# Optimization experiments

Hardware: AMD Instinct MI355X
Metric: run time of the kernel (lower is better)

The kernel has to match this reference:

```python
import jax, jax.numpy as jnp
import numpy as np

H, FF = 4096, 14336   # hidden size, SwiGLU intermediate size
B, S = 4, 2048        # batch, sequence length


def setup_inputs() -> dict:
    key = jax.random.key(0)
    ks = jax.random.split(key, 7)
    x = jax.random.normal(ks[0], (B, S, H), dtype=jnp.float32)
    # Ternary weights: values in {-1, 0, +1}
    gate_t = jax.random.randint(ks[1], (FF, H), -1, 2, dtype=jnp.int32)
    up_t = jax.random.randint(ks[2], (FF, H), -1, 2, dtype=jnp.int32)
    down_t = jax.random.randint(ks[3], (H, FF), -1, 2, dtype=jnp.int32)
    # Per-output-row scales (positive, realistic quantization scale magnitudes)
    gate_s = jax.random.uniform(ks[4], (FF,), jnp.float32, 0.01, 0.1)
    up_s = jax.random.uniform(ks[5], (FF,), jnp.float32, 0.01, 0.1)
    down_s = jax.random.uniform(ks[6], (H,), jnp.float32, 0.01, 0.1)
    return {"x": x, "gate_t": gate_t, "up_t": up_t, "down_t": down_t,
            "gate_s": gate_s, "up_s": up_s, "down_s": down_s}


def reference(x, gate_t, up_t, down_t, gate_s, up_s, down_s):
    # SwiGLU forward with on-the-fly ternary dequant, matching
    # TernaryExpertModule.forward (output_proj=None).
    Bb, Ss, Hh = x.shape
    x_flat = x.reshape(Bb * Ss, Hh)                         # [BS, H]
    gate_w = gate_t.astype(jnp.float32) * gate_s[:, None]   # [FF, H]
    up_w = up_t.astype(jnp.float32) * up_s[:, None]         # [FF, H]
    down_w = down_t.astype(jnp.float32) * down_s[:, None]   # [H, FF]
    gate_out = x_flat @ gate_w.T                            # [BS, FF]
    up_out = x_flat @ up_w.T                                # [BS, FF]
    hidden = jax.nn.silu(gate_out) * up_out                 # [BS, FF]
    out_flat = hidden @ down_w.T                            # [BS, H]
    return out_flat.reshape(Bb, Ss, -1)
```

## Files before the change

kernel.cpp:

```cpp
#include <hip/hip_runtime.h>
#include <stdint.h>

#define H_DIM   4096
#define FF_DIM  14336
#define M_TOK   8192
#define KC1     (H_DIM / 32)
#define KC2     (FF_DIM / 32)
#define NC1     (H_DIM / 64)

typedef unsigned short ushort_t;
typedef __attribute__((ext_vector_type(8)))  short bf16x8;
typedef __attribute__((ext_vector_type(4)))  float f32x4;
typedef __attribute__((ext_vector_type(4)))  int   i32x4;

__device__ __forceinline__ unsigned short f2bf(float f) {
    union { float f; uint32_t u; } v; v.f = f;
    uint32_t r = v.u + 0x7FFFu + ((v.u >> 16) & 1u);
    return (unsigned short)(r >> 16);
}
__device__ __forceinline__ unsigned short t2bf(int v) {
    unsigned int mag = (v & 1) ? 0x3F80u : 0u;
    unsigned int sgn = ((unsigned int)v >> 16) & 0x8000u;
    return (unsigned short)(mag | sgn);
}
__device__ __forceinline__ bf16x8 pack_f8(f32x4 a, f32x4 b) {
    bf16x8 o;
    o[0]=(short)f2bf(a[0]); o[1]=(short)f2bf(a[1]); o[2]=(short)f2bf(a[2]); o[3]=(short)f2bf(a[3]);
    o[4]=(short)f2bf(b[0]); o[5]=(short)f2bf(b[1]); o[6]=(short)f2bf(b[2]); o[7]=(short)f2bf(b[3]);
    return o;
}
__device__ __forceinline__ bf16x8 pack_t8(i32x4 a, i32x4 b) {
    bf16x8 o;
    o[0]=(short)t2bf(a[0]); o[1]=(short)t2bf(a[1]); o[2]=(short)t2bf(a[2]); o[3]=(short)t2bf(a[3]);
    o[4]=(short)t2bf(b[0]); o[5]=(short)t2bf(b[1]); o[6]=(short)t2bf(b[2]); o[7]=(short)t2bf(b[3]);
    return o;
}
__device__ __forceinline__ int pack4(int a, int b, int c, int d) {
    return (a & 255) | ((b & 255) << 8) | ((c & 255) << 16) | ((d & 255) << 24);
}

#define GLDS16(gp, lp) __builtin_amdgcn_global_load_lds( \
    (__attribute__((address_space(1))) void*)(gp),       \
    (__attribute__((address_space(3))) void*)(lp), 16, 0, 0)

#define WAITVM8  asm volatile("s_waitcnt vmcnt(8)" ::: "memory")
#define WAITVM4  asm volatile("s_waitcnt vmcnt(4)" ::: "memory")
#define WAITVM0  asm volatile("s_waitcnt vmcnt(0)" ::: "memory")
#define SBAR     asm volatile("s_barrier" ::: "memory")


template<int K, bool TERN>
__global__ __launch_bounds__(256)
void k_cvt_lds(const void* __restrict__ inv, unsigned short* __restrict__ out) {
    constexpr int KC = K / 32;
    constexpr int CP = K / 64;
    __shared__ int sm[128][68];
    const int b   = blockIdx.x;
    const int t   = b / CP;
    const int cp  = b % CP;
    const int tid = threadIdx.x;
    const int rr  = tid >> 4;
    const int c4  = (tid & 15) * 4;
    const int k0  = cp * 64;

    const int* in = (const int*)inv;
    #pragma unroll
    for (int p = 0; p < 8; ++p) {
        const int row = p * 16 + rr;
        *(i32x4*)&sm[row][c4] = *(const i32x4*)(in + (size_t)(t * 128 + row) * K + k0 + c4);
    }
    __syncthreads();
    #pragma unroll
    for (int p = 0; p < 4; ++p) {
        const int idx = p * 256 + tid;
        const int cc  = idx >> 9;
        const int f   = (idx >> 6) & 7;
        const int l   = idx & 63;
        const int row = f * 16 + (l & 15);
        const int kl  = cc * 32 + (l >> 4) * 8;
        bf16x8 o;
        if (TERN) {
            i32x4 a = *(const i32x4*)&sm[row][kl];
            i32x4 bq = *(const i32x4*)&sm[row][kl + 4];
            o = pack_t8(a, bq);
        } else {
            f32x4 a = *(const f32x4*)&sm[row][kl];
            f32x4 bq = *(const f32x4*)&sm[row][kl + 4];
            o = pack_f8(a, bq);
        }
        *(bf16x8*)(out + (((size_t)t * KC + (cp * 2 + cc)) * 8 + f) * 512 + (size_t)l * 8) = o;
    }
}

__global__ __launch_bounds__(256)
void k_amax(const float* __restrict__ x, float* __restrict__ sx, float* __restrict__ rsx) {
    const int row  = blockIdx.x * 4 + (threadIdx.x >> 6);
    const int lane = threadIdx.x & 63;
    const f32x4* p = (const f32x4*)(x + (size_t)row * H_DIM);
    float m = 0.f;
    #pragma unroll 4
    for (int i = lane; i < H_DIM / 4; i += 64) {
        f32x4 v = p[i];
        m = fmaxf(m, fmaxf(fmaxf(fabsf(v[0]), fabsf(v[1])), fmaxf(fabsf(v[2]), fabsf(v[3]))));
    }
    #pragma unroll
    for (int o = 32; o; o >>= 1) m = fmaxf(m, __shfl_xor(m, o, 64));
    if (lane == 0) {
        sx[row]  = m * (1.f / 127.f);
        rsx[row] = m > 0.f ? 127.f / m : 0.f;
    }
}

template<int K, bool TERN>
__global__ __launch_bounds__(256)
void k_cvt_i8(const void* __restrict__ inv, const float* __restrict__ rsx,
              char* __restrict__ out) {
    constexpr int CP = K / 64;
    __shared__ int sm[128][68];
    const int b   = blockIdx.x;
    const int t   = b / CP;
    const int cp  = b % CP;
    const int tid = threadIdx.x;
    const int rr  = tid >> 4;
    const int c4  = (tid & 15) * 4;

    const int* in = (const int*)inv;
    #pragma unroll
    for (int p = 0; p < 8; ++p) {
        const int row = p * 16 + rr;
        *(i32x4*)&sm[row][c4] = *(const i32x4*)(in + (size_t)(t * 128 + row) * K + cp * 64 + c4);
    }
    __syncthreads();
    #pragma unroll
    for (int p = 0; p < 2; ++p) {
        const int pos = p * 256 + tid;
        const int f = pos >> 6, l = pos & 63;
        const int row = f * 16 + (l & 15);
        const int kb  = (l >> 4) * 16;
        i32x4 o;
        if constexpr (TERN) {
            #pragma unroll
            for (int q = 0; q < 4; ++q)
                o[q] = pack4(sm[row][kb + q * 4], sm[row][kb + q * 4 + 1],
                             sm[row][kb + q * 4 + 2], sm[row][kb + q * 4 + 3]);
        } else {
            const float rs = rsx[t * 128 + row];
            #pragma unroll
            for (int q = 0; q < 4; ++q) {
                const float* fp = (const float*)&sm[row][kb + q * 4];
                o[q] = pack4(__float2int_rn(fp[0] * rs), __float2int_rn(fp[1] * rs),
                             __float2int_rn(fp[2] * rs), __float2int_rn(fp[3] * rs));
            }
        }
        *(i32x4*)(out + ((size_t)t * CP + cp) * 8192 + f * 1024 + (size_t)l * 16) = o;
    }
}

__global__ __launch_bounds__(512, 2)
void k_gemm1_i8(const char* __restrict__ xq,
                const char* __restrict__ gq, const char* __restrict__ uq,
                const float* __restrict__ sxp,
                const float* __restrict__ gs, const float* __restrict__ us,
                ushort_t* __restrict__ hid)
{
    __shared__ char lds[65536];
    const int tid  = threadIdx.x;
    const int lane = tid & 63;
    const int wv   = tid >> 6;
    const int wr   = wv >> 1;
    const int wc   = wv & 1;
    const int l15  = lane & 15;
    const int lq   = lane >> 4;

    const int bid = blockIdx.x;
    const int bmt = bid & 31;
    const int bnt = bid >> 5;

    const char* xa0 = xq + (size_t)(bmt * 2)     * NC1 * 8192;
    const char* xa1 = xq + (size_t)(bmt * 2 + 1) * NC1 * 8192;
    const char* gbb = gq + (size_t)bnt * NC1 * 8192;
    const char* ubb = uq + (size_t)bnt * NC1 * 8192;

    i32x4 accg[4][4] = {};
    i32x4 accu[4][4] = {};

#define STAGE1(h) { char* sl_ = lds + ((h) & 1) * 32768;                     \
    GLDS16(xa0 + (size_t)(h) * 8192 + tid * 16, sl_ + tid * 16);             \
    GLDS16(xa1 + (size_t)(h) * 8192 + tid * 16, sl_ + 8192  + tid * 16);     \
    GLDS16(gbb + (size_t)(h) * 8192 + tid * 16, sl_ + 16384 + tid * 16);     \
    GLDS16(ubb + (size_t)(h) * 8192 + tid * 16, sl_ + 24576 + tid * 16); }

#define G1BODY(WAITOP, DO_STAGE)                                                    \
  {                                                                                 \
    if (DO_STAGE) STAGE1(H + 1);                                                    \
    WAITOP;              \
    SBAR;                                        \
    char* slot = lds + (H & 1) * 32768;                                             \
    const char* Ab = slot + (wr >> 1) * 8192 + ((wr & 1) * 4) * 1024 + lane * 16;   \
    const char* Gb = slot + 16384 + (wc * 4) * 1024 + lane * 16;                    \
    const char* Ub = slot + 24576 + (wc * 4) * 1024 + lane * 16;                    \
    i32x4 af[4], gf[4], uf[4];                                                      \
    _Pragma("unroll")                                                               \
    for (int m = 0; m < 4; m++) af[m] = *(const i32x4*)(Ab + m * 1024);             \
    _Pragma("unroll")                                                               \
    for (int n = 0; n < 4; n++) {                                                   \
        gf[n] = *(const i32x4*)(Gb + n * 1024);                                     \
        uf[n] = *(const i32x4*)(Ub + n * 1024);                                     \
    }                                                                               \
    __builtin_amdgcn_s_setprio(1);                                                  \
    _Pragma("unroll")                                                               \
    for (int m = 0; m < 4; m++)                                                     \
      _Pragma("unroll")                                                             \
      for (int n = 0; n < 4; n++)                                                   \
        accg[m][n] = __builtin_amdgcn_mfma_i32_16x16x64_i8(af[m], gf[n], accg[m][n], 0, 0, 0); \
    _Pragma("unroll")                                                               \
    for (int m = 0; m < 4; m++)                                                     \
      _Pragma("unroll")                                                             \
      for (int n = 0; n < 4; n++)                                                   \
        accu[m][n] = __builtin_amdgcn_mfma_i32_16x16x64_i8(af[m], uf[n], accu[m][n], 0, 0, 0); \
    __builtin_amdgcn_s_setprio(0);                                                  \
    SBAR;                \
  }

    STAGE1(0);
    int H = 0;
    for (; H < NC1 - 1; ++H) G1BODY(WAITVM4, 1);
    G1BODY(WAITVM0, 0);
#undef G1BODY
#undef STAGE1

    const int bm0 = bmt * 256;
    const int bn0 = bnt * 128;
    float sxv[4][4];
    #pragma unroll
    for (int m = 0; m < 4; m++) {
        const int rb = bm0 + wr * 64 + m * 16 + lq * 4;
        #pragma unroll
        for (int r = 0; r < 4; r++) sxv[m][r] = sxp[rb + r];
    }
    #pragma unroll
    for (int n = 0; n < 4; n++) {
        const int gcol = bn0 + wc * 64 + n * 16 + l15;
        const float sg = gs[gcol];
        const float su = us[gcol];
        const int c  = gcol >> 5;
        const int lp = ((gcol & 31) >> 3) * 16;
        const int e  = gcol & 7;
        #pragma unroll
        for (int m = 0; m < 4; m++) {
            const int rb = bm0 + wr * 64 + m * 16 + lq * 4;
            #pragma unroll
            for (int r = 0; r < 4; r++) {
                const int row = rb + r;
                float g = (float)accg[m][n][r] * (sxv[m][r] * sg);
                float u = (float)accu[m][n][r] * (sxv[m][r] * su);
                float hv = g * (1.0f / (1.0f + __expf(-g))) * u;
                const int t = row >> 7;
                const int f = (row >> 4) & 7;
                const int l = (row & 15) + lp;
                hid[(((size_t)t * KC2 + c) * 8 + f) * 512 + l * 8 + e] = f2bf(hv);
            }
        }
    }
}

__global__ __launch_bounds__(512, 2)
void k_gemm2_8p(const ushort_t* __restrict__ hid, const ushort_t* __restrict__ db,
                const float* __restrict__ dsc, float* __restrict__ out)
{
    __shared__ ushort_t lds[65536];
    const int tid  = threadIdx.x;
    const int lane = tid & 63;
    const int wv   = tid >> 6;
    const int wr   = wv >> 2;
    const int wc   = wv & 3;
    const int l15  = lane & 15;
    const int lq   = lane >> 4;

    const int bid = blockIdx.x;
    const int bmt = bid & 31;
    const int bnt = bid >> 5;

    const ushort_t* ha0 = hid + ((size_t)(bmt * 2)     * KC2) * 4096;
    const ushort_t* ha1 = hid + ((size_t)(bmt * 2 + 1) * KC2) * 4096;
    const ushort_t* db0 = db  + ((size_t)(bnt * 2)     * KC2) * 4096;
    const ushort_t* db1 = db  + ((size_t)(bnt * 2 + 1) * KC2) * 4096;

    f32x4 acc[8][4] = {};

    #pragma unroll
    for (int h = 0; h < 3; ++h) {
        ushort_t* sl = lds + h * 16384;
        GLDS16(ha0 + (size_t)h * 4096 + tid * 8, sl + tid * 8);
        GLDS16(ha1 + (size_t)h * 4096 + tid * 8, sl + 4096 + tid * 8);
        GLDS16(db0 + (size_t)h * 4096 + tid * 8, sl + 8192 + tid * 8);
        GLDS16(db1 + (size_t)h * 4096 + tid * 8, sl + 12288 + tid * 8);
    }

#define G2_HALF(WAITOP, DO_ISSUE)                                                  \
  {                                                                                \
    ushort_t* slot = lds + (H & 3) * 16384;                                        \
    const ushort_t* Ab = slot + wr * 4096 + lane * 8;                              \
    const ushort_t* Bb = slot + 8192 + (wc >> 1) * 4096 + ((wc & 1) * 4) * 512 + lane * 8; \
    WAITOP;                                                                        \
    SBAR;                                                                          \
    bf16x8 af[4], bfv[4];                                                          \
    _Pragma("unroll")                                                              \
    for (int m = 0; m < 4; m++) af[m] = *(const bf16x8*)(Ab + m * 512);            \
    _Pragma("unroll")                                                              \
    for (int n = 0; n < 4; n++) bfv[n] = *(const bf16x8*)(Bb + n * 512);           \
    if (DO_ISSUE) {                                                                \
      const int Hp = H + 3;                                                        \
      ushort_t* sp = lds + (Hp & 3) * 16384;                                       \
      GLDS16(ha0 + (size_t)Hp * 4096 + tid * 8, sp + tid * 8);                     \
      GLDS16(ha1 + (size_t)Hp * 4096 + tid * 8, sp + 4096 + tid * 8);              \
    }                                                                              \
    __builtin_amdgcn_s_setprio(1);                                                 \
    _Pragma("unroll")                                                              \
    for (int m = 0; m < 4; m++)                                                    \
      _Pragma("unroll")                                                            \
      for (int n = 0; n < 4; n++)                                                  \
        acc[m][n] = __builtin_amdgcn_mfma_f32_16x16x32_bf16(af[m], bfv[n], acc[m][n], 0, 0, 0); \
    __builtin_amdgcn_s_setprio(0);                                                 \
    SBAR;                                                                          \
    bf16x8 af2[4];                                                                 \
    _Pragma("unroll")                                                              \
    for (int m = 0; m < 4; m++) af2[m] = *(const bf16x8*)(Ab + (4 + m) * 512);     \
    if (DO_ISSUE) {                                                                \
      const int Hp = H + 3;                                                        \
      ushort_t* sp = lds + (Hp & 3) * 16384;                                       \
      GLDS16(db0 + (size_t)Hp * 4096 + tid * 8, sp + 8192 + tid * 8);              \
      GLDS16(db1 + (size_t)Hp * 4096 + tid * 8, sp + 12288 + tid * 8);             \
    }                                                                              \
    __builtin_amdgcn_s_setprio(1);                                                 \
    _Pragma("unroll")                                                              \
    for (int m = 0; m < 4; m++)                                                    \
      _Pragma("unroll")                                                            \
      for (int n = 0; n < 4; n++)                                                  \
        acc[4 + m][n] = __builtin_amdgcn_mfma_f32_16x16x32_bf16(af2[m], bfv[n], acc[4 + m][n], 0, 0, 0); \
    __builtin_amdgcn_s_setprio(0);                                                 \
  }

    int H = 0;
    for (; H < KC2 - 3; ++H) G2_HALF(WAITVM8, 1);
    G2_HALF(WAITVM8, 0); ++H;
    G2_HALF(WAITVM4, 0); ++H;
    G2_HALF(WAITVM0, 0);
#undef G2_HALF

    const int bm0 = bmt * 256;
    const int bn0 = bnt * 256;
    #pragma unroll
    for (int n = 0; n < 4; n++) {
        const int gcol = bn0 + wc * 64 + n * 16 + l15;
        const float sd = dsc[gcol];
        #pragma unroll
        for (int m = 0; m < 8; m++) {
            const int grow = bm0 + wr * 128 + m * 16 + lq * 4;
            #pragma unroll
            for (int r = 0; r < 4; r++)
                out[(size_t)(grow + r) * H_DIM + gcol] = acc[m][n][r] * sd;
        }
    }
}

__device__ __forceinline__ void ds_write_frag(ushort_t* buf, int crow, int ccol,
                                              bf16x8 lo, bf16x8 hi) {
    int f  = crow >> 4;
    int la = (crow & 15) + (((ccol)     & 31) >> 3) * 16;
    int lb = (crow & 15) + (((ccol + 8) & 31) >> 3) * 16;
    *(bf16x8*)&buf[f * 512 + la * 8] = lo;
    *(bf16x8*)&buf[f * 512 + lb * 8] = hi;
}

template<bool PREA>
__global__ __launch_bounds__(256, 2)
void k_gemm1_fb(const float* __restrict__ xf, const ushort_t* __restrict__ xb,
                const int* __restrict__ gt, const int* __restrict__ ut,
                const float* __restrict__ gs, const float* __restrict__ us,
                ushort_t* __restrict__ hid)
{
    __shared__ ushort_t As[4096];
    __shared__ ushort_t Gs[4096];
    __shared__ ushort_t Us[4096];

    const int tid  = threadIdx.x;
    const int lane = tid & 63;
    const int wv   = tid >> 6;
    const int wr   = wv >> 1;
    const int wc   = wv & 1;
    const int l15  = lane & 15;
    const int lq   = lane >> 4;

    const int bid = blockIdx.x;
    const int bmt = bid & 63;
    const int bnt = bid >> 6;
    const int bm0 = bmt * 128;
    const int bn0 = bnt * 128;

    f32x4 accg[4][4] = {};
    f32x4 accu[4][4] = {};

    const ushort_t* pa = PREA ? xb + (size_t)bmt * KC1 * 4096 : nullptr;
    const int crow = tid >> 1;
    const int ccol = (tid & 1) * 16;

    for (int kc = 0; kc < KC1; kc++) {
        __syncthreads();
        const int k0 = kc * 32;
        if constexpr (PREA) {
            GLDS16(pa + tid * 8,        &As[tid * 8]);
            GLDS16(pa + tid * 8 + 2048, &As[tid * 8 + 2048]);
        } else {
            const float* xa = xf + (size_t)(bm0 + crow) * H_DIM + k0 + ccol;
            f32x4 a0 = ((const f32x4*)xa)[0], a1 = ((const f32x4*)xa)[1];
            f32x4 a2 = ((const f32x4*)xa)[2], a3 = ((const f32x4*)xa)[3];
            ds_write_frag(As, crow, ccol, pack_f8(a0, a1), pack_f8(a2, a3));
        }
        {
            const size_t wo = (size_t)(bn0 + crow) * H_DIM + k0 + ccol;
            const i32x4* gp = (const i32x4*)(gt + wo);
            i32x4 g0 = gp[0], g1 = gp[1], g2 = gp[2], g3 = gp[3];
            ds_write_frag(Gs, crow, ccol, pack_t8(g0, g1), pack_t8(g2, g3));
            const i32x4* up = (const i32x4*)(ut + wo);
            i32x4 u0 = up[0], u1 = up[1], u2 = up[2], u3 = up[3];
            ds_write_frag(Us, crow, ccol, pack_t8(u0, u1), pack_t8(u2, u3));
        }
        __syncthreads();

        bf16x8 af[4], gf[4], uf[4];
        #pragma unroll
        for (int m = 0; m < 4; m++)
            af[m] = *(const bf16x8*)&As[(wr * 4 + m) * 512 + lane * 8];
        #pragma unroll
        for (int n = 0; n < 4; n++) {
            gf[n] = *(const bf16x8*)&Gs[(wc * 4 + n) * 512 + lane * 8];
            uf[n] = *(const bf16x8*)&Us[(wc * 4 + n) * 512 + lane * 8];
        }
        #pragma unroll
        for (int m = 0; m < 4; m++)
            #pragma unroll
            for (int n = 0; n < 4; n++) {
                accg[m][n] = __builtin_amdgcn_mfma_f32_16x16x32_bf16(af[m], gf[n], accg[m][n], 0, 0, 0);
                accu[m][n] = __builtin_amdgcn_mfma_f32_16x16x32_bf16(af[m], uf[n], accu[m][n], 0, 0, 0);
            }
        if constexpr (PREA) pa += 4096;
    }

    #pragma unroll
    for (int n = 0; n < 4; n++) {
        const int gcol = bn0 + wc * 64 + n * 16 + l15;
        const float sg = gs[gcol];
        const float su = us[gcol];
        const int c  = gcol >> 5;
        const int lp = ((gcol & 31) >> 3) * 16;
        const int e  = gcol & 7;
        #pragma unroll
        for (int m = 0; m < 4; m++) {
            const int rb = bm0 + wr * 64 + m * 16 + lq * 4;
            #pragma unroll
            for (int r = 0; r < 4; r++) {
                const int row = rb + r;
                float g = accg[m][n][r] * sg;
                float u = accu[m][n][r] * su;
                float hv = g * (1.0f / (1.0f + __expf(-g))) * u;
                const int t = row >> 7;
                const int f = (row >> 4) & 7;
                const int l = (row & 15) + lp;
                hid[(((size_t)t * KC2 + c) * 8 + f) * 512 + l * 8 + e] = f2bf(hv);
            }
        }
    }
}

__global__ __launch_bounds__(256, 2)
void k_gemm2_fb(const ushort_t* __restrict__ hid, const int* __restrict__ dt,
                const float* __restrict__ dsc, float* __restrict__ out)
{
    __shared__ ushort_t As[4096];
    __shared__ ushort_t Bs[4096];

    const int tid  = threadIdx.x;
    const int lane = tid & 63;
    const int wv   = tid >> 6;
    const int wr   = wv >> 1;
    const int wc   = wv & 1;
    const int l15  = lane & 15;
    const int lq   = lane >> 4;

    const int bid = blockIdx.x;
    const int bmt = bid & 63;
    const int bnt = bid >> 6;
    const int bm0 = bmt * 128;
    const int bn0 = bnt * 128;

    f32x4 acc[4][4] = {};
    const ushort_t* pa = hid + (size_t)bmt * KC2 * 4096;
    const int crow = tid >> 1;
    const int ccol = (tid & 1) * 16;

    for (int kc = 0; kc < KC2; kc++) {
        __syncthreads();
        GLDS16(pa + tid * 8,        &As[tid * 8]);
        GLDS16(pa + tid * 8 + 2048, &As[tid * 8 + 2048]);
        {
            const i32x4* dp = (const i32x4*)(dt + (size_t)(bn0 + crow) * FF_DIM + kc * 32 + ccol);
            i32x4 d0 = dp[0], d1 = dp[1], d2 = dp[2], d3 = dp[3];
            ds_write_frag(Bs, crow, ccol, pack_t8(d0, d1), pack_t8(d2, d3));
        }
        __syncthreads();

        bf16x8 af[4], bfr[4];
        #pragma unroll
        for (int m = 0; m < 4; m++)
            af[m] = *(const bf16x8*)&As[(wr * 4 + m) * 512 + lane * 8];
        #pragma unroll
        for (int n = 0; n < 4; n++)
            bfr[n] = *(const bf16x8*)&Bs[(wc * 4 + n) * 512 + lane * 8];
        #pragma unroll
        for (int m = 0; m < 4; m++)
            #pragma unroll
            for (int n = 0; n < 4; n++)
                acc[m][n] = __builtin_amdgcn_mfma_f32_16x16x32_bf16(af[m], bfr[n], acc[m][n], 0, 0, 0);
        pa += 4096;
    }

    #pragma unroll
    for (int n = 0; n < 4; n++) {
        const int gcol = bn0 + wc * 64 + n * 16 + l15;
        const float sd = dsc[gcol];
        #pragma unroll
        for (int m = 0; m < 4; m++) {
            const int grow = bm0 + wr * 64 + m * 16 + lq * 4;
            #pragma unroll
            for (int r = 0; r < 4; r++)
                out[(size_t)(grow + r) * H_DIM + gcol] = acc[m][n][r] * sd;
        }
    }
}

extern "C" void kernel_launch(void* const* d_in, const int* in_sizes, int n_in,
                              void* d_out, int out_size, void* d_ws, size_t ws_size,
                              hipStream_t stream) {
    const float* xf  = (const float*)d_in[0];
    const int*   gt  = (const int*)d_in[1];
    const int*   ut  = (const int*)d_in[2];
    const int*   dt  = (const int*)d_in[3];
    const float* gsc = (const float*)d_in[4];
    const float* usc = (const float*)d_in[5];
    const float* dsc = (const float*)d_in[6];
    float* out = (float*)d_out;

    const size_t HID_B = (size_t)M_TOK * FF_DIM * 2;
    const size_t DB_B  = (size_t)FF_DIM * H_DIM * 2;
    const size_t G8_B  = (size_t)FF_DIM * H_DIM;
    const size_t U8_B  = (size_t)FF_DIM * H_DIM;
    const size_t X8_B  = (size_t)M_TOK * H_DIM;
    const size_t SX_B  = (size_t)M_TOK * 4;
    const size_t XB_B  = (size_t)M_TOK * H_DIM * 2;

    char* base = (char*)d_ws;
    ushort_t* hid = (ushort_t*)base;
    ushort_t* dbp = (ushort_t*)(base + HID_B);
    char*     g8  = base + HID_B + DB_B;
    char*     u8  = g8 + G8_B;
    char*     x8  = u8 + U8_B;
    float*    sxp = (float*)(x8 + X8_B);
    float*    rsx = sxp + M_TOK;
    ushort_t* xbp = (ushort_t*)(base + HID_B);

    const bool has_w  = ws_size >= HID_B + DB_B + G8_B + U8_B + X8_B + 2 * SX_B;
    const bool has_xb = ws_size >= HID_B + XB_B;

    if (has_w) {
        k_amax<<<M_TOK / 4, 256, 0, stream>>>(xf, sxp, rsx);
        k_cvt_i8<H_DIM,  false><<<(M_TOK / 128) * (H_DIM / 64), 256, 0, stream>>>(xf, rsx, x8);
        k_cvt_i8<H_DIM,  true ><<<(FF_DIM / 128) * (H_DIM / 64), 256, 0, stream>>>(gt, nullptr, g8);
        k_cvt_i8<H_DIM,  true ><<<(FF_DIM / 128) * (H_DIM / 64), 256, 0, stream>>>(ut, nullptr, u8);
        k_cvt_lds<FF_DIM, true><<<(H_DIM / 128) * (FF_DIM / 64), 256, 0, stream>>>(dt, dbp);

        k_gemm1_i8<<<32 * 112, 512, 0, stream>>>(x8, g8, u8, sxp, gsc, usc, hid);
        k_gemm2_8p<<<32 * 16, 512, 0, stream>>>(hid, dbp, dsc, out);
    } else {
        const int grid1 = 64 * 112;
        const int grid2 = 64 * 32;
        if (has_xb) {
            k_cvt_lds<H_DIM, false><<<(M_TOK / 128) * (H_DIM / 64), 256, 0, stream>>>(xf, xbp);
            k_gemm1_fb<true><<<grid1, 256, 0, stream>>>(nullptr, xbp, gt, ut, gsc, usc, hid);
        } else {
            k_gemm1_fb<false><<<grid1, 256, 0, stream>>>(xf, nullptr, gt, ut, gsc, usc, hid);
        }
        k_gemm2_fb<<<grid2, 256, 0, stream>>>(hid, dt, dsc, out);
    }
}
```

Measured before the change: 1.778 ms.

## Enlarge gate/up GEMM block tile to 256x256 with a three-stage LDS pipeline

Each int8 gate/up GEMM block now covers 256 output columns instead of 128, with waves arranged 2x4, eight M-fragments per wave, and half the grid. Global-to-LDS staging moves from double buffering to a three-slot ring that prefetches two K-steps ahead, using 144KB of LDS. The aim is better reuse of the activation tile and deeper latency hiding of global loads. In exchange, accumulator register pressure doubles under unchanged launch bounds of (512,2), which risks spills, and the LDS size allows only one block per CU.

```diff
diff --git a/kernel.cpp b/kernel.cpp
--- a/kernel.cpp
+++ b/kernel.cpp
@@ -44,6 +44,7 @@
     (__attribute__((address_space(3))) void*)(lp), 16, 0, 0)
 
 #define WAITVM8  asm volatile("s_waitcnt vmcnt(8)" ::: "memory")
+#define WAITVM6  asm volatile("s_waitcnt vmcnt(6)" ::: "memory")
 #define WAITVM4  asm volatile("s_waitcnt vmcnt(4)" ::: "memory")
 #define WAITVM0  asm volatile("s_waitcnt vmcnt(0)" ::: "memory")
 #define SBAR     asm volatile("s_barrier" ::: "memory")
@@ -163,12 +164,12 @@
                 const float* __restrict__ gs, const float* __restrict__ us,
                 ushort_t* __restrict__ hid)
 {
-    __shared__ char lds[65536];
+    __shared__ char lds[147456];
     const int tid  = threadIdx.x;
     const int lane = tid & 63;
     const int wv   = tid >> 6;
-    const int wr   = wv >> 1;
-    const int wc   = wv & 1;
+    const int wr   = wv >> 2;
+    const int wc   = wv & 3;
     const int l15  = lane & 15;
     const int lq   = lane >> 4;
 
@@ -178,30 +179,33 @@
 
     const char* xa0 = xq + (size_t)(bmt * 2)     * NC1 * 8192;
     const char* xa1 = xq + (size_t)(bmt * 2 + 1) * NC1 * 8192;
-    const char* gbb = gq + (size_t)bnt * NC1 * 8192;
-    const char* ubb = uq + (size_t)bnt * NC1 * 8192;
-
-    i32x4 accg[4][4] = {};
-    i32x4 accu[4][4] = {};
-
-#define STAGE1(h) { char* sl_ = lds + ((h) & 1) * 32768;                     \
-    GLDS16(xa0 + (size_t)(h) * 8192 + tid * 16, sl_ + tid * 16);             \
-    GLDS16(xa1 + (size_t)(h) * 8192 + tid * 16, sl_ + 8192  + tid * 16);     \
-    GLDS16(gbb + (size_t)(h) * 8192 + tid * 16, sl_ + 16384 + tid * 16);     \
-    GLDS16(ubb + (size_t)(h) * 8192 + tid * 16, sl_ + 24576 + tid * 16); }
-
-#define G1BODY(WAITOP, DO_STAGE)                                                    \
+    const char* gb0 = gq + (size_t)(bnt * 2)     * NC1 * 8192;
+    const char* gb1 = gq + (size_t)(bnt * 2 + 1) * NC1 * 8192;
+    const char* ub0 = uq + (size_t)(bnt * 2)     * NC1 * 8192;
+    const char* ub1 = uq + (size_t)(bnt * 2 + 1) * NC1 * 8192;
+
+    i32x4 accg[8][4] = {};
+    i32x4 accu[8][4] = {};
+
+#define STG(h, s) { char* sl_ = lds + (s) * 49152;                            \
+    GLDS16(xa0 + (size_t)(h) * 8192 + tid * 16, sl_ + tid * 16);              \
+    GLDS16(xa1 + (size_t)(h) * 8192 + tid * 16, sl_ + 8192  + tid * 16);      \
+    GLDS16(gb0 + (size_t)(h) * 8192 + tid * 16, sl_ + 16384 + tid * 16);      \
+    GLDS16(gb1 + (size_t)(h) * 8192 + tid * 16, sl_ + 24576 + tid * 16);      \
+    GLDS16(ub0 + (size_t)(h) * 8192 + tid * 16, sl_ + 32768 + tid * 16);      \
+    GLDS16(ub1 + (size_t)(h) * 8192 + tid * 16, sl_ + 40960 + tid * 16); }
+
+#define G1BODY(WAITOP, SLOT)                                                        \
   {                                                                                 \
-    if (DO_STAGE) STAGE1(H + 1);                                                    \
-    WAITOP;              \
+    WAITOP;                                             \
     SBAR;                                        \
-    char* slot = lds + (H & 1) * 32768;                                             \
-    const char* Ab = slot + (wr >> 1) * 8192 + ((wr & 1) * 4) * 1024 + lane * 16;   \
-    const char* Gb = slot + 16384 + (wc * 4) * 1024 + lane * 16;                    \
-    const char* Ub = slot + 24576 + (wc * 4) * 1024 + lane * 16;                    \
-    i32x4 af[4], gf[4], uf[4];                                                      \
+    char* slot = lds + (SLOT) * 49152;                                              \
+    const char* Ab = slot + wr * 8192 + lane * 16;                                  \
+    const char* Gb = slot + 16384 + (wc >> 1) * 8192 + ((wc & 1) * 4) * 1024 + lane * 16; \
+    const char* Ub = Gb + 16384;                                                    \
+    i32x4 af[8], gf[4], uf[4];                                                      \
     _Pragma("unroll")                                                               \
-    for (int m = 0; m < 4; m++) af[m] = *(const i32x4*)(Ab + m * 1024);             \
+    for (int m = 0; m < 8; m++) af[m] = *(const i32x4*)(Ab + m * 1024);             \
     _Pragma("unroll")                                                               \
     for (int n = 0; n < 4; n++) {                                                   \
         gf[n] = *(const i32x4*)(Gb + n * 1024);                                     \
@@ -209,32 +213,38 @@
     }                                                                               \
     __builtin_amdgcn_s_setprio(1);                                                  \
     _Pragma("unroll")                                                               \
-    for (int m = 0; m < 4; m++)                                                     \
+    for (int m = 0; m < 8; m++)                                                     \
       _Pragma("unroll")                                                             \
       for (int n = 0; n < 4; n++)                                                   \
         accg[m][n] = __builtin_amdgcn_mfma_i32_16x16x64_i8(af[m], gf[n], accg[m][n], 0, 0, 0); \
     _Pragma("unroll")                                                               \
-    for (int m = 0; m < 4; m++)                                                     \
+    for (int m = 0; m < 8; m++)                                                     \
       _Pragma("unroll")                                                             \
       for (int n = 0; n < 4; n++)                                                   \
         accu[m][n] = __builtin_amdgcn_mfma_i32_16x16x64_i8(af[m], uf[n], accu[m][n], 0, 0, 0); \
     __builtin_amdgcn_s_setprio(0);                                                  \
-    SBAR;                \
+    SBAR;                         \
   }
 
-    STAGE1(0);
-    int H = 0;
-    for (; H < NC1 - 1; ++H) G1BODY(WAITVM4, 1);
-    G1BODY(WAITVM0, 0);
+    STG(0, 0); STG(1, 1);
+    int s0 = 0;
+    for (int H = 0; H < NC1 - 2; ++H) {
+        const int sn = (s0 + 2 >= 3) ? s0 - 1 : s0 + 2;
+        G1BODY(WAITVM6, s0);
+        STG(H + 2, sn);
+        s0 = (s0 + 1 >= 3) ? 0 : s0 + 1;
+    }
+    G1BODY(WAITVM6, s0);  s0 = (s0 + 1 >= 3) ? 0 : s0 + 1;
+    G1BODY(WAITVM0, s0);
 #undef G1BODY
-#undef STAGE1
+#undef STG
 
     const int bm0 = bmt * 256;
-    const int bn0 = bnt * 128;
-    float sxv[4][4];
-    #pragma unroll
-    for (int m = 0; m < 4; m++) {
-        const int rb = bm0 + wr * 64 + m * 16 + lq * 4;
+    const int bn0 = bnt * 256;
+    float sxv[8][4];
+    #pragma unroll
+    for (int m = 0; m < 8; m++) {
+        const int rb = bm0 + wr * 128 + m * 16 + lq * 4;
         #pragma unroll
         for (int r = 0; r < 4; r++) sxv[m][r] = sxp[rb + r];
     }
@@ -247,8 +257,8 @@
         const int lp = ((gcol & 31) >> 3) * 16;
         const int e  = gcol & 7;
         #pragma unroll
-        for (int m = 0; m < 4; m++) {
-            const int rb = bm0 + wr * 64 + m * 16 + lq * 4;
+        for (int m = 0; m < 8; m++) {
+            const int rb = bm0 + wr * 128 + m * 16 + lq * 4;
             #pragma unroll
             for (int r = 0; r < 4; r++) {
                 const int row = rb + r;
@@ -579,7 +589,7 @@
         k_cvt_i8<H_DIM,  true ><<<(FF_DIM / 128) * (H_DIM / 64), 256, 0, stream>>>(ut, nullptr, u8);
         k_cvt_lds<FF_DIM, true><<<(H_DIM / 128) * (FF_DIM / 64), 256, 0, stream>>>(dt, dbp);
 
-        k_gemm1_i8<<<32 * 112, 512, 0, stream>>>(x8, g8, u8, sxp, gsc, usc, hid);
+        k_gemm1_i8<<<32 * 56, 512, 0, stream>>>(x8, g8, u8, sxp, gsc, usc, hid);
         k_gemm2_8p<<<32 * 16, 512, 0, stream>>>(hid, dbp, dsc, out);
     } else {
         const int grid1 = 64 * 112;
```

New measurement: 6.787 ms. +281.6%, slower.
